# Kernel tuning notes

Measured on AMD Instinct MI355X. Metric: run time of the kernel, lower is better.

The kernel has to match this reference:

```python
import jax, jax.numpy as jnp
import numpy as np

B, A, T, N, H = 16, 32, 64, 8, 256
E, D, F = 8, 32, 128  # heads, key_dim, ff_dim
LN_EPS = 1e-6


def setup_inputs() -> dict:
    key = jax.random.key(0)
    ks = jax.random.split(key, 8)
    s = 0.02
    return {
        'hidden_vecs': jax.random.normal(ks[0], (B, A, T, N, H), jnp.float32),
        'scene_hidden_vec': jax.random.normal(ks[1], (B, 1, H), jnp.float32),
        'Wq': jax.random.normal(ks[2], (H, E, D), jnp.float32) * s,
        'bq': jnp.zeros((E, D), jnp.float32),
        'Wk': jax.random.normal(ks[3], (H, E, D), jnp.float32) * s,
        'bk': jnp.zeros((E, D), jnp.float32),
        'Wv': jax.random.normal(ks[4], (H, E, D), jnp.float32) * s,
        'bv': jnp.zeros((E, D), jnp.float32),
        'Wo': jax.random.normal(ks[5], (E, D, H), jnp.float32) * s,
        'bo': jnp.zeros((H,), jnp.float32),
        'ln1_g': jnp.ones((H,), jnp.float32),
        'ln1_b': jnp.zeros((H,), jnp.float32),
        'W1': jax.random.normal(ks[6], (H, F), jnp.float32) * s,
        'b1': jnp.zeros((F,), jnp.float32),
        'W2': jax.random.normal(ks[7], (F, H), jnp.float32) * s,
        'b2': jnp.zeros((H,), jnp.float32),
        'ln2_g': jnp.ones((H,), jnp.float32),
        'ln2_b': jnp.zeros((H,), jnp.float32),
    }


def _layernorm(x, g, b):
    mu = jnp.mean(x, axis=-1, keepdims=True)
    var = jnp.mean(jnp.square(x - mu), axis=-1, keepdims=True)
    return (x - mu) * jax.lax.rsqrt(var + LN_EPS) * g + b


def reference(hidden_vecs, scene_hidden_vec, Wq, bq, Wk, bk, Wv, bv, Wo, bo,
              ln1_g, ln1_b, W1, b1, W2, b2, ln2_g, ln2_b):
    # Cross-attention: query = per-token hidden vecs (query length 1 along axis 4),
    # key/value = single scene token, broadcast instead of materializing tf.tile.
    scale = 1.0 / jnp.sqrt(jnp.asarray(D, hidden_vecs.dtype))
    # q: [b,a,t,m,e,d]; k,v: [b,s,e,d] with s=1
    q = jnp.einsum('batmh,hed->batmed', hidden_vecs, Wq) + bq
    k = jnp.einsum('bsh,hed->bsed', scene_hidden_vec, Wk) + bk
    v = jnp.einsum('bsh,hed->bsed', scene_hidden_vec, Wv) + bv
    scores = jnp.einsum('batmed,bsed->batmes', q, k) * scale  # [b,a,t,m,e,1]
    p = jax.nn.softmax(scores, axis=-1)  # all ones (single key), kept for fidelity
    attn = jnp.einsum('batmes,bsed->batmed', p, v)
    attn_out = jnp.einsum('batmed,edh->batmh', attn, Wo) + bo
    # attention scores as returned by keras MHA: [b,a,t,m,heads,q_len=1,kv_len=1]
    attn_score = p[..., None, :]
    x1 = _layernorm(attn_out + hidden_vecs, ln1_g, ln1_b)
    ff = jax.nn.relu(jnp.einsum('batmh,hf->batmf', x1, W1) + b1)
    ff = jnp.einsum('batmf,fh->batmh', ff, W2) + b2
    out = _layernorm(ff + x1, ln2_g, ln2_b)
    return out, attn_score
```

## Files before the change

### kernel.cpp

```cpp
#include <hip/hip_runtime.h>
#include <hip/hip_bf16.h>


typedef __attribute__((ext_vector_type(4))) float f32x4;
typedef __attribute__((ext_vector_type(8))) short s16x8;

#define TILE 32
#define LDX 260
#define LDF 136
#define LN_EPS 1e-6f

__device__ __forceinline__ short f2bs(float f) {
  unsigned int u = __builtin_bit_cast(unsigned int, f);
  unsigned int r = (u + 0x7FFFu + ((u >> 16) & 1u)) >> 16;
  return (short)r;
}

__global__ void attn_vec_kernel(const float* __restrict__ scene,
                                const float* __restrict__ Wv, const float* __restrict__ bv,
                                const float* __restrict__ Wo, const float* __restrict__ bo,
                                float* __restrict__ attn_vec) {
  __shared__ float sc[256];
  __shared__ float vv[256];
  const int b = blockIdx.x, t = threadIdx.x;
  sc[t] = scene[b * 256 + t];
  __syncthreads();
  float acc = bv[t];
  #pragma unroll 4
  for (int h = 0; h < 256; ++h) acc += sc[h] * Wv[h * 256 + t];
  vv[t] = acc;
  __syncthreads();
  float o = bo[t];
  #pragma unroll 4
  for (int ed = 0; ed < 256; ++ed) o += vv[ed] * Wo[ed * 256 + t];
  attn_vec[b * 256 + t] = o;
}

__global__ void pack_kernel(const float* __restrict__ W1, const float* __restrict__ W2,
                            unsigned short* __restrict__ W1p, unsigned short* __restrict__ W2p) {
  const int tid = blockIdx.x * 256 + threadIdx.x;
  const int i = tid & 32767;
  const int j = i & 7, l = (i >> 3) & 63, g = i >> 9;
  const int krow = (l >> 4) * 8 + j, c = l & 15;
  if (tid < 32768) {
    const int ks = g >> 3, nt = g & 7;
    W1p[i] = (unsigned short)f2bs(W1[(ks * 32 + krow) * 128 + nt * 16 + c]);
  } else {
    const int ks = g >> 4, nt = g & 15;
    W2p[i] = (unsigned short)f2bs(W2[(ks * 32 + krow) * 256 + nt * 16 + c]);
  }
}

__global__ void fill_ones_kernel(f32x4* __restrict__ p) {
  const int i = blockIdx.x * 256 + threadIdx.x;
  p[i] = (f32x4){1.f, 1.f, 1.f, 1.f};
}

__launch_bounds__(256)
__global__ void main_kernel(const float* __restrict__ hidden,
                            const float* __restrict__ attn_vec,
                            const float* __restrict__ ln1g, const float* __restrict__ ln1b,
                            const unsigned short* __restrict__ W1p, const float* __restrict__ b1,
                            const unsigned short* __restrict__ W2p, const float* __restrict__ b2,
                            const float* __restrict__ ln2g, const float* __restrict__ ln2b,
                            float* __restrict__ out) {
  __shared__ float xs[TILE * LDX];
  __shared__ unsigned short ffs[TILE * LDF];
  __shared__ float red[TILE * 4 * 2];
  __shared__ float murs[TILE * 2];

  const int tid  = threadIdx.x;
  const int lane = tid & 63;
  const int w    = tid >> 6;
  const int l15  = lane & 15, l4 = lane >> 4;
  const long base_tok = (long)blockIdx.x * TILE;
  const float* hp = hidden + base_tok * 256;
  float* outp = out + base_tok * 256;

  s16x8 b1f[8][2];
  #pragma unroll
  for (int ks = 0; ks < 8; ++ks)
    #pragma unroll
    for (int ntl = 0; ntl < 2; ++ntl)
      b1f[ks][ntl] = *(const s16x8*)(W1p + (((ks * 8) + (w * 2 + ntl)) * 64 + lane) * 8);

  float b1c[2];
  #pragma unroll
  for (int ntl = 0; ntl < 2; ++ntl) b1c[ntl] = b1[w * 32 + ntl * 16 + l15];
  float b2c[4], g2c[4], be2c[4];
  #pragma unroll
  for (int ntl = 0; ntl < 4; ++ntl) {
    const int c = w * 64 + ntl * 16 + l15;
    b2c[ntl] = b2[c]; g2c[ntl] = ln2g[c]; be2c[ntl] = ln2b[c];
  }

  const int csub = tid & 63;
  const int bidx = (int)(base_tok >> 14);
  const f32x4 av  = *(const f32x4*)(attn_vec + bidx * 256 + csub * 4);
  const f32x4 g1  = *(const f32x4*)(ln1g + csub * 4);
  const f32x4 be1 = *(const f32x4*)(ln1b + csub * 4);

  f32x4 xv[8];
  #pragma unroll
  for (int i = 0; i < 8; ++i) {
    const int token = i * 4 + w;
    xv[i] = *(const f32x4*)(hp + token * 256 + csub * 4) + av;
  }
  #pragma unroll
  for (int i = 0; i < 8; ++i) {
    float s = xv[i][0] + xv[i][1] + xv[i][2] + xv[i][3];
    float q = xv[i][0]*xv[i][0] + xv[i][1]*xv[i][1] + xv[i][2]*xv[i][2] + xv[i][3]*xv[i][3];
    #pragma unroll
    for (int d = 1; d < 64; d <<= 1) { s += __shfl_xor(s, d); q += __shfl_xor(q, d); }
    const float mu = s * (1.f / 256.f);
    const float rs = rsqrtf(q * (1.f / 256.f) - mu * mu + LN_EPS);
    const f32x4 x1 = (xv[i] - mu) * rs * g1 + be1;
    const int token = i * 4 + w;
    *(f32x4*)&xs[token * LDX + csub * 4] = x1;
  }
  __syncthreads();

  f32x4 acc1[2][2] = {};
  #pragma unroll
  for (int ks = 0; ks < 8; ++ks) {
    #pragma unroll
    for (int m = 0; m < 2; ++m) {
      const float* ap = &xs[(m * 16 + l15) * LDX + ks * 32 + l4 * 8];
      const f32x4 a0 = *(const f32x4*)ap;
      const f32x4 a1 = *(const f32x4*)(ap + 4);
      s16x8 af;
      af[0]=f2bs(a0[0]); af[1]=f2bs(a0[1]); af[2]=f2bs(a0[2]); af[3]=f2bs(a0[3]);
      af[4]=f2bs(a1[0]); af[5]=f2bs(a1[1]); af[6]=f2bs(a1[2]); af[7]=f2bs(a1[3]);
      #pragma unroll
      for (int ntl = 0; ntl < 2; ++ntl)
        acc1[m][ntl] = __builtin_amdgcn_mfma_f32_16x16x32_bf16(af, b1f[ks][ntl], acc1[m][ntl], 0, 0, 0);
    }
  }
  #pragma unroll
  for (int m = 0; m < 2; ++m)
    #pragma unroll
    for (int ntl = 0; ntl < 2; ++ntl) {
      const int col = w * 32 + ntl * 16 + l15;
      #pragma unroll
      for (int r = 0; r < 4; ++r) {
        const float z = fmaxf(acc1[m][ntl][r] + b1c[ntl], 0.f);
        ffs[(m * 16 + l4 * 4 + r) * LDF + col] = (unsigned short)f2bs(z);
      }
    }

  s16x8 b2f[4][4];
  #pragma unroll
  for (int ks = 0; ks < 4; ++ks)
    #pragma unroll
    for (int ntl = 0; ntl < 4; ++ntl)
      b2f[ks][ntl] = *(const s16x8*)(W2p + (((ks * 16) + (w * 4 + ntl)) * 64 + lane) * 8);
  __syncthreads();

  f32x4 acc2[2][4] = {};
  #pragma unroll
  for (int ks = 0; ks < 4; ++ks) {
    #pragma unroll
    for (int m = 0; m < 2; ++m) {
      const s16x8 af = *(const s16x8*)&ffs[(m * 16 + l15) * LDF + ks * 32 + l4 * 8];
      #pragma unroll
      for (int ntl = 0; ntl < 4; ++ntl)
        acc2[m][ntl] = __builtin_amdgcn_mfma_f32_16x16x32_bf16(af, b2f[ks][ntl], acc2[m][ntl], 0, 0, 0);
    }
  }

  #pragma unroll
  for (int m = 0; m < 2; ++m)
    #pragma unroll
    for (int ntl = 0; ntl < 4; ++ntl) {
      const int col = w * 64 + ntl * 16 + l15;
      #pragma unroll
      for (int r = 0; r < 4; ++r) {
        const int row = m * 16 + l4 * 4 + r;
        acc2[m][ntl][r] += b2c[ntl] + xs[row * LDX + col];
      }
    }
  #pragma unroll
  for (int m = 0; m < 2; ++m)
    #pragma unroll
    for (int r = 0; r < 4; ++r) {
      float s = 0.f, q = 0.f;
      #pragma unroll
      for (int ntl = 0; ntl < 4; ++ntl) { const float z = acc2[m][ntl][r]; s += z; q += z * z; }
      #pragma unroll
      for (int d = 1; d < 16; d <<= 1) { s += __shfl_xor(s, d); q += __shfl_xor(q, d); }
      if (l15 == 0) {
        const int row = m * 16 + l4 * 4 + r;
        red[(row * 4 + w) * 2 + 0] = s;
        red[(row * 4 + w) * 2 + 1] = q;
      }
    }
  __syncthreads();
  if (tid < TILE) {
    float s = 0.f, q = 0.f;
    #pragma unroll
    for (int ww = 0; ww < 4; ++ww) { s += red[(tid * 4 + ww) * 2]; q += red[(tid * 4 + ww) * 2 + 1]; }
    const float mu = s * (1.f / 256.f);
    murs[tid * 2 + 0] = mu;
    murs[tid * 2 + 1] = rsqrtf(q * (1.f / 256.f) - mu * mu + LN_EPS);
  }
  __syncthreads();
  #pragma unroll
  for (int m = 0; m < 2; ++m)
    #pragma unroll
    for (int r = 0; r < 4; ++r) {
      const int row = m * 16 + l4 * 4 + r;
      const float mu = murs[row * 2], rs = murs[row * 2 + 1];
      #pragma unroll
      for (int ntl = 0; ntl < 4; ++ntl) {
        const int col = w * 64 + ntl * 16 + l15;
        xs[row * LDX + col] = (acc2[m][ntl][r] - mu) * rs * g2c[ntl] + be2c[ntl];
      }
    }
  __syncthreads();
  #pragma unroll
  for (int i = 0; i < 8; ++i) {
    const int token = i * 4 + w;
    *(f32x4*)(outp + token * 256 + csub * 4) = *(const f32x4*)&xs[token * LDX + csub * 4];
  }
}

extern "C" void kernel_launch(void* const* d_in, const int* in_sizes, int n_in,
                              void* d_out, int out_size, void* d_ws, size_t ws_size,
                              hipStream_t stream) {
  const float* hidden = (const float*)d_in[0];
  const float* scene  = (const float*)d_in[1];
  const float* Wv   = (const float*)d_in[6];
  const float* bv   = (const float*)d_in[7];
  const float* Wo   = (const float*)d_in[8];
  const float* bo   = (const float*)d_in[9];
  const float* ln1g = (const float*)d_in[10];
  const float* ln1b = (const float*)d_in[11];
  const float* W1   = (const float*)d_in[12];
  const float* b1   = (const float*)d_in[13];
  const float* W2   = (const float*)d_in[14];
  const float* b2   = (const float*)d_in[15];
  const float* ln2g = (const float*)d_in[16];
  const float* ln2b = (const float*)d_in[17];
  float* out = (float*)d_out;

  float* attn_vec = (float*)d_ws;
  unsigned short* W1p = (unsigned short*)((char*)d_ws + 16384);
  unsigned short* W2p = (unsigned short*)((char*)d_ws + 16384 + 65536);

  attn_vec_kernel<<<16, 256, 0, stream>>>(scene, Wv, bv, Wo, bo, attn_vec);
  pack_kernel<<<256, 256, 0, stream>>>(W1, W2, W1p, W2p);
  fill_ones_kernel<<<2048, 256, 0, stream>>>((f32x4*)(out + 67108864));
  main_kernel<<<8192, 256, 0, stream>>>(hidden, attn_vec, ln1g, ln1b,
                                        W1p, b1, W2p, b2, ln2g, ln2b, out);
}
```

Baseline: 588.5 us.

## Merge prep kernels, store LN1 output as bf16, cut registers for occupancy

Three small setup kernels become one prep kernel, saving two launches. The main kernel stores the LayerNorm-1 output in shared memory as bf16 rather than fp32, roughly halving that LDS footprint and removing repeated conversions in the first GEMM loop. Weight fragments now load in two halves and launch bounds request 5 blocks per CU, cutting register pressure to raise occupancy. The LN2 reduction is recomputed per thread without an extra barrier, and output goes straight to global memory with strided scalar stores instead of coalesced vector stores via LDS; the residual now uses the bf16-rounded x1, which loses some precision.

```diff
diff --git a/kernel.cpp b/kernel.cpp
--- a/kernel.cpp
+++ b/kernel.cpp
@@ -4,10 +4,12 @@
 
 typedef __attribute__((ext_vector_type(4))) float f32x4;
 typedef __attribute__((ext_vector_type(8))) short s16x8;
+typedef __attribute__((ext_vector_type(4))) short s16x4;
 
 #define TILE 32
-#define LDX 260
-#define LDF 136
+#define LDXS 264
+#define LDF  136
+#define LDR  12
 #define LN_EPS 1e-6f
 
 __device__ __forceinline__ short f2bs(float f) {
@@ -15,48 +17,53 @@
   unsigned int r = (u + 0x7FFFu + ((u >> 16) & 1u)) >> 16;
   return (short)r;
 }
-
-__global__ void attn_vec_kernel(const float* __restrict__ scene,
-                                const float* __restrict__ Wv, const float* __restrict__ bv,
-                                const float* __restrict__ Wo, const float* __restrict__ bo,
-                                float* __restrict__ attn_vec) {
+__device__ __forceinline__ float bs2f(unsigned short s) {
+  unsigned int u = ((unsigned int)s) << 16;
+  return __builtin_bit_cast(float, u);
+}
+
+__global__ void prep_kernel(const float* __restrict__ scene,
+                            const float* __restrict__ Wv, const float* __restrict__ bv,
+                            const float* __restrict__ Wo, const float* __restrict__ bo,
+                            const float* __restrict__ W1, const float* __restrict__ W2,
+                            float* __restrict__ attn_vec,
+                            unsigned short* __restrict__ W1p, unsigned short* __restrict__ W2p,
+                            f32x4* __restrict__ score) {
   __shared__ float sc[256];
   __shared__ float vv[256];
-  const int b = blockIdx.x, t = threadIdx.x;
-  sc[t] = scene[b * 256 + t];
-  __syncthreads();
-  float acc = bv[t];
-  #pragma unroll 4
-  for (int h = 0; h < 256; ++h) acc += sc[h] * Wv[h * 256 + t];
-  vv[t] = acc;
-  __syncthreads();
-  float o = bo[t];
-  #pragma unroll 4
-  for (int ed = 0; ed < 256; ++ed) o += vv[ed] * Wo[ed * 256 + t];
-  attn_vec[b * 256 + t] = o;
-}
-
-__global__ void pack_kernel(const float* __restrict__ W1, const float* __restrict__ W2,
-                            unsigned short* __restrict__ W1p, unsigned short* __restrict__ W2p) {
-  const int tid = blockIdx.x * 256 + threadIdx.x;
-  const int i = tid & 32767;
-  const int j = i & 7, l = (i >> 3) & 63, g = i >> 9;
-  const int krow = (l >> 4) * 8 + j, c = l & 15;
-  if (tid < 32768) {
-    const int ks = g >> 3, nt = g & 7;
-    W1p[i] = (unsigned short)f2bs(W1[(ks * 32 + krow) * 128 + nt * 16 + c]);
+  const int bid = blockIdx.x, t = threadIdx.x;
+  if (bid < 16) {
+    const int b = bid;
+    sc[t] = scene[b * 256 + t];
+    __syncthreads();
+    float acc = bv[t];
+    #pragma unroll 8
+    for (int h = 0; h < 256; ++h) acc += sc[h] * Wv[h * 256 + t];
+    vv[t] = acc;
+    __syncthreads();
+    float o = bo[t];
+    #pragma unroll 8
+    for (int ed = 0; ed < 256; ++ed) o += vv[ed] * Wo[ed * 256 + t];
+    attn_vec[b * 256 + t] = o;
+  } else if (bid < 272) {
+    const int tid = (bid - 16) * 256 + t;
+    const int i = tid & 32767;
+    const int j = i & 7, l = (i >> 3) & 63, g = i >> 9;
+    const int krow = (l >> 4) * 8 + j, c = l & 15;
+    if (tid < 32768) {
+      const int ks = g >> 3, nt = g & 7;
+      W1p[i] = (unsigned short)f2bs(W1[(ks * 32 + krow) * 128 + nt * 16 + c]);
+    } else {
+      const int ks = g >> 4, nt = g & 15;
+      W2p[i] = (unsigned short)f2bs(W2[(ks * 32 + krow) * 256 + nt * 16 + c]);
+    }
   } else {
-    const int ks = g >> 4, nt = g & 15;
-    W2p[i] = (unsigned short)f2bs(W2[(ks * 32 + krow) * 256 + nt * 16 + c]);
+    const int i = (bid - 272) * 256 + t;
+    score[i] = (f32x4){1.f, 1.f, 1.f, 1.f};
   }
 }
 
-__global__ void fill_ones_kernel(f32x4* __restrict__ p) {
-  const int i = blockIdx.x * 256 + threadIdx.x;
-  p[i] = (f32x4){1.f, 1.f, 1.f, 1.f};
-}
-
-__launch_bounds__(256)
+__launch_bounds__(256, 5)
 __global__ void main_kernel(const float* __restrict__ hidden,
                             const float* __restrict__ attn_vec,
                             const float* __restrict__ ln1g, const float* __restrict__ ln1b,
@@ -64,10 +71,9 @@
                             const unsigned short* __restrict__ W2p, const float* __restrict__ b2,
                             const float* __restrict__ ln2g, const float* __restrict__ ln2b,
                             float* __restrict__ out) {
-  __shared__ float xs[TILE * LDX];
+  __shared__ unsigned short xs[TILE * LDXS];
   __shared__ unsigned short ffs[TILE * LDF];
-  __shared__ float red[TILE * 4 * 2];
-  __shared__ float murs[TILE * 2];
+  __shared__ float red[TILE * LDR];
 
   const int tid  = threadIdx.x;
   const int lane = tid & 63;
@@ -77,9 +83,18 @@
   const float* hp = hidden + base_tok * 256;
   float* outp = out + base_tok * 256;
 
-  s16x8 b1f[8][2];
-  #pragma unroll
-  for (int ks = 0; ks < 8; ++ks)
+  const int bidx = (int)(base_tok >> 14);
+  const f32x4 av  = *(const f32x4*)(attn_vec + bidx * 256 + lane * 4);
+  const f32x4 g1  = *(const f32x4*)(ln1g + lane * 4);
+  const f32x4 be1 = *(const f32x4*)(ln1b + lane * 4);
+  f32x4 xv[8];
+  #pragma unroll
+  for (int i = 0; i < 8; ++i)
+    xv[i] = *(const f32x4*)(hp + (i * 4 + w) * 256 + lane * 4);
+
+  s16x8 b1f[4][2];
+  #pragma unroll
+  for (int ks = 0; ks < 4; ++ks)
     #pragma unroll
     for (int ntl = 0; ntl < 2; ++ntl)
       b1f[ks][ntl] = *(const s16x8*)(W1p + (((ks * 8) + (w * 2 + ntl)) * 64 + lane) * 8);
@@ -94,48 +109,48 @@
     b2c[ntl] = b2[c]; g2c[ntl] = ln2g[c]; be2c[ntl] = ln2b[c];
   }
 
-  const int csub = tid & 63;
-  const int bidx = (int)(base_tok >> 14);
-  const f32x4 av  = *(const f32x4*)(attn_vec + bidx * 256 + csub * 4);
-  const f32x4 g1  = *(const f32x4*)(ln1g + csub * 4);
-  const f32x4 be1 = *(const f32x4*)(ln1b + csub * 4);
-
-  f32x4 xv[8];
   #pragma unroll
   for (int i = 0; i < 8; ++i) {
     const int token = i * 4 + w;
-    xv[i] = *(const f32x4*)(hp + token * 256 + csub * 4) + av;
-  }
-  #pragma unroll
-  for (int i = 0; i < 8; ++i) {
-    float s = xv[i][0] + xv[i][1] + xv[i][2] + xv[i][3];
-    float q = xv[i][0]*xv[i][0] + xv[i][1]*xv[i][1] + xv[i][2]*xv[i][2] + xv[i][3]*xv[i][3];
+    const f32x4 x = xv[i] + av;
+    float s = x[0] + x[1] + x[2] + x[3];
+    float q = x[0]*x[0] + x[1]*x[1] + x[2]*x[2] + x[3]*x[3];
     #pragma unroll
     for (int d = 1; d < 64; d <<= 1) { s += __shfl_xor(s, d); q += __shfl_xor(q, d); }
     const float mu = s * (1.f / 256.f);
     const float rs = rsqrtf(q * (1.f / 256.f) - mu * mu + LN_EPS);
-    const f32x4 x1 = (xv[i] - mu) * rs * g1 + be1;
-    const int token = i * 4 + w;
-    *(f32x4*)&xs[token * LDX + csub * 4] = x1;
+    const f32x4 x1 = (x - mu) * rs * g1 + be1;
+    s16x4 xb;
+    xb[0] = f2bs(x1[0]); xb[1] = f2bs(x1[1]); xb[2] = f2bs(x1[2]); xb[3] = f2bs(x1[3]);
+    *(s16x4*)&xs[token * LDXS + lane * 4] = xb;
   }
   __syncthreads();
 
   f32x4 acc1[2][2] = {};
   #pragma unroll
-  for (int ks = 0; ks < 8; ++ks) {
-    #pragma unroll
-    for (int m = 0; m < 2; ++m) {
-      const float* ap = &xs[(m * 16 + l15) * LDX + ks * 32 + l4 * 8];
-      const f32x4 a0 = *(const f32x4*)ap;
-      const f32x4 a1 = *(const f32x4*)(ap + 4);
-      s16x8 af;
-      af[0]=f2bs(a0[0]); af[1]=f2bs(a0[1]); af[2]=f2bs(a0[2]); af[3]=f2bs(a0[3]);
-      af[4]=f2bs(a1[0]); af[5]=f2bs(a1[1]); af[6]=f2bs(a1[2]); af[7]=f2bs(a1[3]);
+  for (int ks = 0; ks < 4; ++ks)
+    #pragma unroll
+    for (int m = 0; m < 2; ++m) {
+      const s16x8 af = *(const s16x8*)&xs[(m * 16 + l15) * LDXS + ks * 32 + l4 * 8];
       #pragma unroll
       for (int ntl = 0; ntl < 2; ++ntl)
         acc1[m][ntl] = __builtin_amdgcn_mfma_f32_16x16x32_bf16(af, b1f[ks][ntl], acc1[m][ntl], 0, 0, 0);
     }
-  }
+  #pragma unroll
+  for (int ks = 0; ks < 4; ++ks)
+    #pragma unroll
+    for (int ntl = 0; ntl < 2; ++ntl)
+      b1f[ks][ntl] = *(const s16x8*)(W1p + ((((ks + 4) * 8) + (w * 2 + ntl)) * 64 + lane) * 8);
+  #pragma unroll
+  for (int ks = 0; ks < 4; ++ks)
+    #pragma unroll
+    for (int m = 0; m < 2; ++m) {
+      const s16x8 af = *(const s16x8*)&xs[(m * 16 + l15) * LDXS + (ks + 4) * 32 + l4 * 8];
+      #pragma unroll
+      for (int ntl = 0; ntl < 2; ++ntl)
+        acc1[m][ntl] = __builtin_amdgcn_mfma_f32_16x16x32_bf16(af, b1f[ks][ntl], acc1[m][ntl], 0, 0, 0);
+    }
+
   #pragma unroll
   for (int m = 0; m < 2; ++m)
     #pragma unroll
@@ -148,9 +163,9 @@
       }
     }
 
-  s16x8 b2f[4][4];
-  #pragma unroll
-  for (int ks = 0; ks < 4; ++ks)
+  s16x8 b2f[2][4];
+  #pragma unroll
+  for (int ks = 0; ks < 2; ++ks)
     #pragma unroll
     for (int ntl = 0; ntl < 4; ++ntl)
       b2f[ks][ntl] = *(const s16x8*)(W2p + (((ks * 16) + (w * 4 + ntl)) * 64 + lane) * 8);
@@ -158,7 +173,7 @@
 
   f32x4 acc2[2][4] = {};
   #pragma unroll
-  for (int ks = 0; ks < 4; ++ks) {
+  for (int ks = 0; ks < 2; ++ks)
     #pragma unroll
     for (int m = 0; m < 2; ++m) {
       const s16x8 af = *(const s16x8*)&ffs[(m * 16 + l15) * LDF + ks * 32 + l4 * 8];
@@ -166,7 +181,20 @@
       for (int ntl = 0; ntl < 4; ++ntl)
         acc2[m][ntl] = __builtin_amdgcn_mfma_f32_16x16x32_bf16(af, b2f[ks][ntl], acc2[m][ntl], 0, 0, 0);
     }
-  }
+  #pragma unroll
+  for (int ks = 0; ks < 2; ++ks)
+    #pragma unroll
+    for (int ntl = 0; ntl < 4; ++ntl)
+      b2f[ks][ntl] = *(const s16x8*)(W2p + ((((ks + 2) * 16) + (w * 4 + ntl)) * 64 + lane) * 8);
+  #pragma unroll
+  for (int ks = 0; ks < 2; ++ks)
+    #pragma unroll
+    for (int m = 0; m < 2; ++m) {
+      const s16x8 af = *(const s16x8*)&ffs[(m * 16 + l15) * LDF + (ks + 2) * 32 + l4 * 8];
+      #pragma unroll
+      for (int ntl = 0; ntl < 4; ++ntl)
+        acc2[m][ntl] = __builtin_amdgcn_mfma_f32_16x16x32_bf16(af, b2f[ks][ntl], acc2[m][ntl], 0, 0, 0);
+    }
 
   #pragma unroll
   for (int m = 0; m < 2; ++m)
@@ -176,7 +204,7 @@
       #pragma unroll
       for (int r = 0; r < 4; ++r) {
         const int row = m * 16 + l4 * 4 + r;
-        acc2[m][ntl][r] += b2c[ntl] + xs[row * LDX + col];
+        acc2[m][ntl][r] += b2c[ntl] + bs2f(xs[row * LDXS + col]);
       }
     }
   #pragma unroll
@@ -190,38 +218,28 @@
       for (int d = 1; d < 16; d <<= 1) { s += __shfl_xor(s, d); q += __shfl_xor(q, d); }
       if (l15 == 0) {
         const int row = m * 16 + l4 * 4 + r;
-        red[(row * 4 + w) * 2 + 0] = s;
-        red[(row * 4 + w) * 2 + 1] = q;
-      }
-    }
-  __syncthreads();
-  if (tid < TILE) {
-    float s = 0.f, q = 0.f;
-    #pragma unroll
-    for (int ww = 0; ww < 4; ++ww) { s += red[(tid * 4 + ww) * 2]; q += red[(tid * 4 + ww) * 2 + 1]; }
-    const float mu = s * (1.f / 256.f);
-    murs[tid * 2 + 0] = mu;
-    murs[tid * 2 + 1] = rsqrtf(q * (1.f / 256.f) - mu * mu + LN_EPS);
-  }
+        red[row * LDR + w * 2 + 0] = s;
+        red[row * LDR + w * 2 + 1] = q;
+      }
+    }
   __syncthreads();
   #pragma unroll
   for (int m = 0; m < 2; ++m)
     #pragma unroll
     for (int r = 0; r < 4; ++r) {
       const int row = m * 16 + l4 * 4 + r;
-      const float mu = murs[row * 2], rs = murs[row * 2 + 1];
+      const f32x4 a = *(const f32x4*)&red[row * LDR];
+      const f32x4 b = *(const f32x4*)&red[row * LDR + 4];
+      const float s = a[0] + a[2] + b[0] + b[2];
+      const float q = a[1] + a[3] + b[1] + b[3];
+      const float mu = s * (1.f / 256.f);
+      const float rs = rsqrtf(q * (1.f / 256.f) - mu * mu + LN_EPS);
       #pragma unroll
       for (int ntl = 0; ntl < 4; ++ntl) {
         const int col = w * 64 + ntl * 16 + l15;
-        xs[row * LDX + col] = (acc2[m][ntl][r] - mu) * rs * g2c[ntl] + be2c[ntl];
-      }
-    }
-  __syncthreads();
-  #pragma unroll
-  for (int i = 0; i < 8; ++i) {
-    const int token = i * 4 + w;
-    *(f32x4*)(outp + token * 256 + csub * 4) = *(const f32x4*)&xs[token * LDX + csub * 4];
-  }
+        outp[row * 256 + col] = (acc2[m][ntl][r] - mu) * rs * g2c[ntl] + be2c[ntl];
+      }
+    }
 }
 
 extern "C" void kernel_launch(void* const* d_in, const int* in_sizes, int n_in,
@@ -247,9 +265,9 @@
   unsigned short* W1p = (unsigned short*)((char*)d_ws + 16384);
   unsigned short* W2p = (unsigned short*)((char*)d_ws + 16384 + 65536);
 
-  attn_vec_kernel<<<16, 256, 0, stream>>>(scene, Wv, bv, Wo, bo, attn_vec);
-  pack_kernel<<<256, 256, 0, stream>>>(W1, W2, W1p, W2p);
-  fill_ones_kernel<<<2048, 256, 0, stream>>>((f32x4*)(out + 67108864));
+  prep_kernel<<<2320, 256, 0, stream>>>(scene, Wv, bv, Wo, bo, W1, W2,
+                                        attn_vec, W1p, W2p,
+                                        (f32x4*)(out + 67108864));
   main_kernel<<<8192, 256, 0, stream>>>(hidden, attn_vec, ln1g, ln1b,
                                         W1p, b1, W2p, b2, ln2g, ln2b, out);
 }
```

Measured after the change: 554.1 us. 5.8% less time.
